# Performance work log

Hardware: AMD Instinct MI355X
Metric: run time of the kernel (lower is better)

The kernel has to match this reference:

```python
import jax, jax.numpy as jnp
import numpy as np

D_MODEL = 2048
N_HEAD = 16
SEM_DIM = 1024
GEO_DIM = 1024
ATTN_DIM = 2048
ROPE_BASE = 10000.0


def _rope(x, base=ROPE_BASE):
    # x: [B, H, S, d] with even d; GPT-NeoX rotate-half convention
    S, d = x.shape[-2], x.shape[-1]
    inv_freq = 1.0 / (base ** (jnp.arange(0, d, 2, dtype=jnp.float32) / d))
    t = jnp.arange(S, dtype=jnp.float32)
    freqs = jnp.einsum('s,f->sf', t, inv_freq)  # [S, d/2]
    cos, sin = jnp.cos(freqs), jnp.sin(freqs)
    x1, x2 = x[..., : d // 2], x[..., d // 2 :]
    return jnp.concatenate([x1 * cos - x2 * sin, x1 * sin + x2 * cos], axis=-1).astype(x.dtype)


def _split_heads(y, H):
    B, S, dim = y.shape
    return y.reshape(B, S, H, dim // H).transpose(0, 2, 1, 3)  # [B,H,S,hd]


def setup_inputs() -> dict:
    key = jax.random.key(0)
    ks = jax.random.split(key, 7)
    B, S = 2, 2048
    sd = 0.02
    return {
        'x': jax.random.normal(ks[0], (B, S, D_MODEL), dtype=jnp.float32),
        'Wq_sem': jax.random.normal(ks[1], (SEM_DIM, D_MODEL), dtype=jnp.float32) * sd,
        'Wk_sem': jax.random.normal(ks[2], (SEM_DIM, D_MODEL), dtype=jnp.float32) * sd,
        'Wq_geo': jax.random.normal(ks[3], (GEO_DIM, D_MODEL), dtype=jnp.float32) * sd,
        'Wk_geo': jax.random.normal(ks[4], (GEO_DIM, D_MODEL), dtype=jnp.float32) * sd,
        'Wv': jax.random.normal(ks[5], (ATTN_DIM, D_MODEL), dtype=jnp.float32) * sd,
        'Wo': jax.random.normal(ks[6], (D_MODEL, ATTN_DIM), dtype=jnp.float32) * sd,
    }


def reference(x, Wq_sem, Wk_sem, Wq_geo, Wk_geo, Wv, Wo):
    B, S, _ = x.shape
    H = N_HEAD
    # decoupled projections (nn.Linear: y = x @ W.T)
    q_sem = _split_heads(x @ Wq_sem.T, H)  # [B,H,S,64]
    k_sem = _split_heads(x @ Wk_sem.T, H)
    q_geo = _rope(_split_heads(x @ Wq_geo.T, H))  # RoPE only on geo part
    k_geo = _rope(_split_heads(x @ Wk_geo.T, H))
    v = _split_heads(x @ Wv.T, H)  # [B,H,S,128]
    # concatenated decoupled q/k -> single fused score (fp32), SDPA default scale
    q = jnp.concatenate([q_sem, q_geo], axis=-1)
    k = jnp.concatenate([k_sem, k_geo], axis=-1)
    scale = 1.0 / jnp.sqrt(jnp.asarray(q.shape[-1], dtype=jnp.float32))
    scores = jnp.einsum('bhqd,bhkd->bhqk', q, k).astype(jnp.float32) * scale
    causal = jnp.tril(jnp.ones((S, S), dtype=bool))
    scores = jnp.where(causal, scores, jnp.finfo(jnp.float32).min)
    attn = jax.nn.softmax(scores, axis=-1).astype(v.dtype)
    out = jnp.einsum('bhqk,bhkd->bhqd', attn, v)  # [B,H,S,128]
    out = out.transpose(0, 2, 1, 3).reshape(B, S, ATTN_DIM)
    return out @ Wo.T  # [B,S,d_model]
```

## Files before the change

kernel.cpp:

```cpp
#include <hip/hip_runtime.h>
#include <cstdint>
#include <cstddef>

typedef unsigned short u16;
typedef __attribute__((ext_vector_type(8))) short bf16x8;
typedef __attribute__((ext_vector_type(4))) float f32x4;

#define MFMA32(a, b, c) __builtin_amdgcn_mfma_f32_16x16x32_bf16(a, b, c, 0, 0, 0)

__device__ __forceinline__ u16 f2b(float f) {
  union { float f; unsigned u; } v; v.f = f;
  unsigned u = v.u;
  return (u16)((u + 0x7fffu + ((u >> 16) & 1u)) >> 16);
}
__device__ __forceinline__ float b2f(u16 h) {
  union { unsigned u; float f; } v; v.u = ((unsigned)h) << 16;
  return v.f;
}

__device__ __forceinline__ void g2l16(const void* g, void* l) {
  __builtin_amdgcn_global_load_lds((__attribute__((address_space(1))) void*)(g),
                                   (__attribute__((address_space(3))) void*)(l), 16, 0, 0);
}

__global__ __launch_bounds__(256) void cast_all(const float* __restrict__ x,
                                                const float* __restrict__ W0,
                                                const float* __restrict__ W1,
                                                const float* __restrict__ W2,
                                                const float* __restrict__ W3,
                                                const float* __restrict__ Wv,
                                                const float* __restrict__ Wo,
                                                u16* __restrict__ xb,
                                                u16* __restrict__ Wall,
                                                u16* __restrict__ Wob) {
  const int blk = blockIdx.x;
  const float* src;
  u16* dst;
  int li;
  if (blk < 8192) {
    src = x; dst = xb; li = blk * 256 + threadIdx.x;
  } else if (blk < 16384) {
    const int s = (blk - 8192) >> 11;
    src = s == 0 ? W0 : s == 1 ? W1 : s == 2 ? W2 : W3;
    dst = Wall + (size_t)s * 2097152;
    li = ((blk - 8192) & 2047) * 256 + threadIdx.x;
  } else if (blk < 20480) {
    src = Wv; dst = Wall + (size_t)4 * 2097152;
    li = (blk - 16384) * 256 + threadIdx.x;
  } else {
    src = Wo; dst = Wob;
    li = (blk - 20480) * 256 + threadIdx.x;
  }
  float4 v = ((const float4*)src)[li];
  ushort4 r;
  r.x = f2b(v.x); r.y = f2b(v.y); r.z = f2b(v.z); r.w = f2b(v.w);
  ((ushort4*)dst)[li] = r;
}

template <bool BF16_OUT>
__global__ __launch_bounds__(256) void gemm_bt(const u16* __restrict__ A,
                                               const u16* __restrict__ B,
                                               void* __restrict__ C, int N, int K) {
  __shared__ u16 As[128 * 64];
  __shared__ u16 Bs[128 * 64];
  const int tid = threadIdx.x;
  const int wid = tid >> 6;
  const int lane = tid & 63;
  const int lm = lane & 15;
  const int quad = lane >> 4;
  const int r3 = lm & 7;
  const int wm = (wid & 1) * 64;
  const int wn = (wid >> 1) * 64;
  const int bm = blockIdx.y * 128;
  const int bn = blockIdx.x * 128;

  const u16* Ab = A + (size_t)bm * K;
  const u16* Bb = B + (size_t)bn * K;

  f32x4 zero = {0.f, 0.f, 0.f, 0.f};
  f32x4 acc[4][4];
#pragma unroll
  for (int i = 0; i < 4; ++i)
#pragma unroll
    for (int j = 0; j < 4; ++j) acc[i][j] = zero;

  for (int k0 = 0; k0 < K; k0 += 64) {
#pragma unroll
    for (int it = 0; it < 4; ++it) {
      int c = it * 256 + tid;
      int rg = c >> 6, rw = (c >> 3) & 7, u = c & 7;
      int row = rg * 8 + rw;
      int chd = u ^ rw;
      g2l16(Ab + (size_t)row * K + k0 + chd * 8, As + c * 8);
      g2l16(Bb + (size_t)row * K + k0 + chd * 8, Bs + c * 8);
    }
    __syncthreads();
#pragma unroll
    for (int ks = 0; ks < 2; ++ks) {
      bf16x8 a[4], b[4];
      int chd = ks * 4 + quad;
#pragma unroll
      for (int i = 0; i < 4; ++i) {
        int row = wm + i * 16 + lm;
        a[i] = *(const bf16x8*)(As + (((row >> 3) * 64 + r3 * 8 + (chd ^ r3)) * 8));
      }
#pragma unroll
      for (int j = 0; j < 4; ++j) {
        int row = wn + j * 16 + lm;
        b[j] = *(const bf16x8*)(Bs + (((row >> 3) * 64 + r3 * 8 + (chd ^ r3)) * 8));
      }
#pragma unroll
      for (int i = 0; i < 4; ++i)
#pragma unroll
        for (int j = 0; j < 4; ++j)
          acc[i][j] = MFMA32(a[i], b[j], acc[i][j]);
    }
    __syncthreads();
  }

#pragma unroll
  for (int i = 0; i < 4; ++i)
#pragma unroll
    for (int j = 0; j < 4; ++j)
#pragma unroll
      for (int r = 0; r < 4; ++r) {
        int row = bm + wm + i * 16 + quad * 4 + r;
        int col = bn + wn + j * 16 + lm;
        float v = acc[i][j][r];
        if (BF16_OUT)
          ((u16*)C)[(size_t)row * N + col] = f2b(v);
        else
          ((float*)C)[(size_t)row * N + col] = v;
      }
}

__global__ __launch_bounds__(256) void gemm_qkv(const u16* __restrict__ A,
                                                const u16* __restrict__ B,
                                                u16* __restrict__ Qb,
                                                u16* __restrict__ Kb,
                                                u16* __restrict__ VT) {
  constexpr int K = 2048;
  const float SC = 0.12751744f;
  __shared__ u16 sh[16384];
  u16* As = sh;
  u16* Bs = sh + 8192;
  const int tid = threadIdx.x;
  const int wid = tid >> 6;
  const int lane = tid & 63;
  const int lm = lane & 15;
  const int quad = lane >> 4;
  const int r3 = lm & 7;
  const int wm = (wid & 1) * 64;
  const int wn = (wid >> 1) * 64;
  const int bm = blockIdx.y * 128;
  const int bn = blockIdx.x * 128;

  const u16* Ab = A + (size_t)bm * K;
  const u16* Bb = B + (size_t)bn * K;

  f32x4 zero = {0.f, 0.f, 0.f, 0.f};
  f32x4 acc[4][4];
#pragma unroll
  for (int i = 0; i < 4; ++i)
#pragma unroll
    for (int j = 0; j < 4; ++j) acc[i][j] = zero;

  for (int k0 = 0; k0 < K; k0 += 64) {
#pragma unroll
    for (int it = 0; it < 4; ++it) {
      int c = it * 256 + tid;
      int rg = c >> 6, rw = (c >> 3) & 7, u = c & 7;
      int row = rg * 8 + rw;
      int chd = u ^ rw;
      g2l16(Ab + (size_t)row * K + k0 + chd * 8, As + c * 8);
      g2l16(Bb + (size_t)row * K + k0 + chd * 8, Bs + c * 8);
    }
    __syncthreads();
#pragma unroll
    for (int ks = 0; ks < 2; ++ks) {
      bf16x8 a[4], b[4];
      int chd = ks * 4 + quad;
#pragma unroll
      for (int i = 0; i < 4; ++i) {
        int row = wm + i * 16 + lm;
        a[i] = *(const bf16x8*)(As + (((row >> 3) * 64 + r3 * 8 + (chd ^ r3)) * 8));
      }
#pragma unroll
      for (int j = 0; j < 4; ++j) {
        int row = wn + j * 16 + lm;
        b[j] = *(const bf16x8*)(Bs + (((row >> 3) * 64 + r3 * 8 + (chd ^ r3)) * 8));
      }
#pragma unroll
      for (int i = 0; i < 4; ++i)
#pragma unroll
        for (int j = 0; j < 4; ++j)
          acc[i][j] = MFMA32(a[i], b[j], acc[i][j]);
    }
    __syncthreads();
  }

  const int seg = bn >> 10;
  const int b = bm >> 11;
  const int sbase = bm & 2047;
  const int h = ((bn + wn) >> 6) & 15;
  const size_t bhQ = (size_t)b * 16 + h;

  if (seg < 2) {
    u16* dst = (seg == 0) ? Qb : Kb;
    const float sc = (seg == 0) ? SC : 1.0f;
#pragma unroll
    for (int i = 0; i < 4; ++i)
#pragma unroll
      for (int r = 0; r < 4; ++r) {
        const int s = sbase + wm + i * 16 + quad * 4 + r;
        u16* base = dst + (bhQ * 2048 + s) * 128;
#pragma unroll
        for (int j = 0; j < 4; ++j) {
          const int d = (wn + j * 16 + lm) & 63;
          base[d] = f2b(acc[i][j][r] * sc);
        }
      }
  } else if (seg < 4) {
    u16* dst = (seg == 2) ? Qb : Kb;
    const float sc = (seg == 2) ? SC : 1.0f;
    const float inv0 = __powf(10000.0f, -(float)(2 * lm) * (1.0f / 64.0f));
    const float inv1 = __powf(10000.0f, -(float)(2 * (16 + lm)) * (1.0f / 64.0f));
#pragma unroll
    for (int i = 0; i < 4; ++i)
#pragma unroll
      for (int r = 0; r < 4; ++r) {
        const int s = sbase + wm + i * 16 + quad * 4 + r;
        float sn0, cs0, sn1, cs1;
        __sincosf((float)s * inv0, &sn0, &cs0);
        __sincosf((float)s * inv1, &sn1, &cs1);
        const float x1a = acc[i][0][r], x2a = acc[i][2][r];
        const float x1b = acc[i][1][r], x2b = acc[i][3][r];
        u16* base = dst + (bhQ * 2048 + s) * 128 + 64;
        base[lm]      = f2b((x1a * cs0 - x2a * sn0) * sc);
        base[16 + lm] = f2b((x1b * cs1 - x2b * sn1) * sc);
        base[32 + lm] = f2b((x1a * sn0 + x2a * cs0) * sc);
        base[48 + lm] = f2b((x1b * sn1 + x2b * cs1) * sc);
      }
  } else {
    const int hv = (bn - 4096) >> 7;
    const size_t bh = (size_t)b * 16 + hv;
#pragma unroll
    for (int i = 0; i < 4; ++i)
#pragma unroll
      for (int r = 0; r < 4; ++r) {
        const int sr = wm + i * 16 + quad * 4 + r;
#pragma unroll
        for (int j = 0; j < 4; ++j) {
          const int d = wn + j * 16 + lm;
          sh[d * 128 + (((sr >> 3) ^ (d & 7)) << 3) + (sr & 7)] = f2b(acc[i][j][r]);
        }
      }
    __syncthreads();
#pragma unroll
    for (int it = 0; it < 8; ++it) {
      const int idx = it * 256 + tid;
      const int d = idx >> 4;
      const int ch = idx & 15;
      bf16x8 v = *(const bf16x8*)(sh + d * 128 + ((ch ^ (d & 7)) << 3));
      *(bf16x8*)(VT + (bh * 128 + d) * 2048 + sbase + ch * 8) = v;
    }
  }
}

__global__ __launch_bounds__(256, 3) void attn_v9(const u16* __restrict__ Q,
                                                  const u16* __restrict__ K,
                                                  const u16* __restrict__ VT,
                                                  u16* __restrict__ O) {
  constexpr int S = 2048;
  constexpr int D = 128;
  __shared__ u16 Ks[64 * 128];
  __shared__ u16 Vs[128 * 64];
  __shared__ u16 Ps[64 * 72];
  const int linear = blockIdx.x + (blockIdx.y << 4);
  const int xcd = linear & 7;
  const int slot = linear >> 3;
  const int bh = (xcd << 2) + (slot >> 4);
  const int bx = slot & 15;
  const int b = bh >> 4, h = bh & 15;
  const int tid = threadIdx.x, wid = tid >> 6, lane = tid & 63;
  const int lm = lane & 15, quad = lane >> 4;
  const int rx = lm & 7;
  const int wrow = wid * 16;

  const u16* Kbh = K + (size_t)bh * S * D;
  const u16* Vbh = VT + (size_t)bh * D * S;

  const bf16x8 vones = {16256, 16256, 16256, 16256, 16256, 16256, 16256, 16256};

#pragma unroll 1
  for (int pass = 0; pass < 2; ++pass) {
    const int qt = pass == 0 ? bx : 31 - bx;

    bf16x8 aq[4];
#pragma unroll
    for (int ks = 0; ks < 4; ++ks)
      aq[ks] = *(const bf16x8*)(Q + ((size_t)bh * S + (size_t)qt * 64 + wrow + lm) * D +
                                ks * 32 + quad * 8);

    f32x4 zero = {0.f, 0.f, 0.f, 0.f};
    f32x4 lsum = zero;
    f32x4 oacc[8];
#pragma unroll
    for (int t = 0; t < 8; ++t) oacc[t] = zero;

#pragma unroll 1
    for (int kt = 0; kt <= qt; ++kt) {
      __syncthreads();
      const u16* Kt = Kbh + (size_t)kt * 64 * D;
      const u16* Vt = Vbh + (size_t)kt * 64;
#pragma unroll
      for (int it = 0; it < 4; ++it) {
        int c = it * 256 + tid;
        int row = c >> 4, u = c & 15;
        g2l16(Kt + (size_t)row * 128 + (size_t)(u ^ (row & 7)) * 8, Ks + c * 8);
      }
#pragma unroll
      for (int it = 0; it < 4; ++it) {
        int c = it * 256 + tid;
        int row = c >> 3, u = c & 7;
        g2l16(Vt + (size_t)row * S + (size_t)(u ^ (row & 7)) * 8, Vs + c * 8);
      }
      __syncthreads();

      f32x4 sc[4];
#pragma unroll
      for (int j = 0; j < 4; ++j) sc[j] = zero;
      __builtin_amdgcn_s_setprio(1);
#pragma unroll
      for (int ks = 0; ks < 4; ++ks) {
        const int kc = ks * 4 + quad;
#pragma unroll
        for (int j = 0; j < 4; ++j) {
          bf16x8 bk = *(const bf16x8*)(Ks + (((j * 16 + lm) * 16 + (kc ^ rx)) * 8));
          sc[j] = MFMA32(aq[ks], bk, sc[j]);
        }
      }
      __builtin_amdgcn_s_setprio(0);

      const bool diag = (kt == qt);
#pragma unroll
      for (int r = 0; r < 4; ++r) {
        const int qcol = wrow + quad * 4 + r;
        const int prow = (wrow + quad * 4 + r) * 72;
#pragma unroll
        for (int j = 0; j < 4; ++j) {
          float p = __builtin_amdgcn_exp2f(fminf(sc[j][r], 30.0f));
          if (diag && (j * 16 + lm > qcol)) p = 0.f;
          Ps[prow + j * 16 + lm] = f2b(p);
        }
      }

      __builtin_amdgcn_s_setprio(1);
#pragma unroll
      for (int ks = 0; ks < 2; ++ks) {
        bf16x8 ap = *(const bf16x8*)(Ps + (wrow + lm) * 72 + ks * 32 + quad * 8);
        const int kc = ks * 4 + quad;
        lsum = MFMA32(ap, vones, lsum);
#pragma unroll
        for (int t = 0; t < 8; ++t) {
          bf16x8 bv = *(const bf16x8*)(Vs + (((t * 16 + lm) * 8 + (kc ^ rx)) * 8));
          oacc[t] = MFMA32(ap, bv, oacc[t]);
        }
      }
      __builtin_amdgcn_s_setprio(0);
    }

#pragma unroll
    for (int r = 0; r < 4; ++r) {
      float inv = 1.0f / lsum[r];
      const int srow = qt * 64 + wrow + quad * 4 + r;
      u16* Orow = O + ((size_t)b * S + srow) * 2048 + h * 128;
#pragma unroll
      for (int t = 0; t < 8; ++t) Orow[t * 16 + lm] = f2b(oacc[t][r] * inv);
    }
  }
}

extern "C" void kernel_launch(void* const* d_in, const int* in_sizes, int n_in,
                              void* d_out, int out_size, void* d_ws, size_t ws_size,
                              hipStream_t stream) {
  const float* x      = (const float*)d_in[0];
  const float* Wq_sem = (const float*)d_in[1];
  const float* Wk_sem = (const float*)d_in[2];
  const float* Wq_geo = (const float*)d_in[3];
  const float* Wk_geo = (const float*)d_in[4];
  const float* Wv     = (const float*)d_in[5];
  const float* Wo     = (const float*)d_in[6];

  char* ws = (char*)d_ws;
  u16* xb   = (u16*)(ws);
  u16* Wall = (u16*)(ws + 16777216);
  u16* Wob  = (u16*)(ws + 16777216 + 25165824);
  u16* Qb   = (u16*)(ws + 16777216 + 25165824 + 8388608);
  u16* Ob   = Wall;
  u16* Kb   = (u16*)d_out;
  u16* VT   = (u16*)((char*)d_out + 16777216);

  cast_all<<<24576, 256, 0, stream>>>(x, Wq_sem, Wk_sem, Wq_geo, Wk_geo, Wv, Wo,
                                      xb, Wall, Wob);

  gemm_qkv<<<dim3(48, 32), 256, 0, stream>>>(xb, Wall, Qb, Kb, VT);

  attn_v9<<<dim3(16, 32), 256, 0, stream>>>(Qb, Kb, VT, Ob);

  gemm_bt<false><<<dim3(16, 32), 256, 0, stream>>>(Ob, Wob, d_out, 2048, 2048);
}
```

Before: 359.4 us.

## Process both paired query tiles in one KV sweep to share K/V loads

The attention kernel used to make two sequential passes, one per query tile (bx and 31-bx), and reloaded the K/V tiles from global memory in each pass. Now a single loop over KV tiles serves both query tiles: the later tile B uses every KV tile and the earlier tile A only the tiles up to its causal limit, so each K/V tile is staged into LDS once. The cost is twice the accumulator registers (two sets of 8 f32x4 output accumulators plus two Q fragments) and a second P buffer in LDS, which under launch_bounds(256,3) may cause spills or lower occupancy.

```diff
diff --git a/kernel.cpp b/kernel.cpp
--- a/kernel.cpp
+++ b/kernel.cpp
@@ -267,15 +267,16 @@
   }
 }
 
-__global__ __launch_bounds__(256, 3) void attn_v9(const u16* __restrict__ Q,
-                                                  const u16* __restrict__ K,
-                                                  const u16* __restrict__ VT,
-                                                  u16* __restrict__ O) {
+__global__ __launch_bounds__(256, 3) void attn_v10(const u16* __restrict__ Q,
+                                                   const u16* __restrict__ K,
+                                                   const u16* __restrict__ VT,
+                                                   u16* __restrict__ O) {
   constexpr int S = 2048;
   constexpr int D = 128;
   __shared__ u16 Ks[64 * 128];
   __shared__ u16 Vs[128 * 64];
-  __shared__ u16 Ps[64 * 72];
+  __shared__ u16 PsA[64 * 72];
+  __shared__ u16 PsB[64 * 72];
   const int linear = blockIdx.x + (blockIdx.y << 4);
   const int xcd = linear & 7;
   const int slot = linear >> 3;
@@ -287,46 +288,51 @@
   const int rx = lm & 7;
   const int wrow = wid * 16;
 
+  const int qtA = bx;
+  const int qtB = 31 - bx;
+
   const u16* Kbh = K + (size_t)bh * S * D;
   const u16* Vbh = VT + (size_t)bh * D * S;
 
   const bf16x8 vones = {16256, 16256, 16256, 16256, 16256, 16256, 16256, 16256};
 
+  bf16x8 aqA[4], aqB[4];
+#pragma unroll
+  for (int ks = 0; ks < 4; ++ks) {
+    aqA[ks] = *(const bf16x8*)(Q + ((size_t)bh * S + (size_t)qtA * 64 + wrow + lm) * D +
+                               ks * 32 + quad * 8);
+    aqB[ks] = *(const bf16x8*)(Q + ((size_t)bh * S + (size_t)qtB * 64 + wrow + lm) * D +
+                               ks * 32 + quad * 8);
+  }
+
+  f32x4 zero = {0.f, 0.f, 0.f, 0.f};
+  f32x4 lsumA = zero, lsumB = zero;
+  f32x4 oaccA[8], oaccB[8];
+#pragma unroll
+  for (int t = 0; t < 8; ++t) { oaccA[t] = zero; oaccB[t] = zero; }
+
 #pragma unroll 1
-  for (int pass = 0; pass < 2; ++pass) {
-    const int qt = pass == 0 ? bx : 31 - bx;
-
-    bf16x8 aq[4];
-#pragma unroll
-    for (int ks = 0; ks < 4; ++ks)
-      aq[ks] = *(const bf16x8*)(Q + ((size_t)bh * S + (size_t)qt * 64 + wrow + lm) * D +
-                                ks * 32 + quad * 8);
-
-    f32x4 zero = {0.f, 0.f, 0.f, 0.f};
-    f32x4 lsum = zero;
-    f32x4 oacc[8];
-#pragma unroll
-    for (int t = 0; t < 8; ++t) oacc[t] = zero;
-
-#pragma unroll 1
-    for (int kt = 0; kt <= qt; ++kt) {
-      __syncthreads();
-      const u16* Kt = Kbh + (size_t)kt * 64 * D;
-      const u16* Vt = Vbh + (size_t)kt * 64;
-#pragma unroll
-      for (int it = 0; it < 4; ++it) {
-        int c = it * 256 + tid;
-        int row = c >> 4, u = c & 15;
-        g2l16(Kt + (size_t)row * 128 + (size_t)(u ^ (row & 7)) * 8, Ks + c * 8);
-      }
-#pragma unroll
-      for (int it = 0; it < 4; ++it) {
-        int c = it * 256 + tid;
-        int row = c >> 3, u = c & 7;
-        g2l16(Vt + (size_t)row * S + (size_t)(u ^ (row & 7)) * 8, Vs + c * 8);
-      }
-      __syncthreads();
-
+  for (int kt = 0; kt <= qtB; ++kt) {
+    __syncthreads();
+    const u16* Kt = Kbh + (size_t)kt * 64 * D;
+    const u16* Vt = Vbh + (size_t)kt * 64;
+#pragma unroll
+    for (int it = 0; it < 4; ++it) {
+      int c = it * 256 + tid;
+      int row = c >> 4, u = c & 15;
+      g2l16(Kt + (size_t)row * 128 + (size_t)(u ^ (row & 7)) * 8, Ks + c * 8);
+    }
+#pragma unroll
+    for (int it = 0; it < 4; ++it) {
+      int c = it * 256 + tid;
+      int row = c >> 3, u = c & 7;
+      g2l16(Vt + (size_t)row * S + (size_t)(u ^ (row & 7)) * 8, Vs + c * 8);
+    }
+    __syncthreads();
+
+    const bool doA = (kt <= qtA);
+
+    {
       f32x4 sc[4];
 #pragma unroll
       for (int j = 0; j < 4; ++j) sc[j] = zero;
@@ -337,12 +343,11 @@
 #pragma unroll
         for (int j = 0; j < 4; ++j) {
           bf16x8 bk = *(const bf16x8*)(Ks + (((j * 16 + lm) * 16 + (kc ^ rx)) * 8));
-          sc[j] = MFMA32(aq[ks], bk, sc[j]);
+          sc[j] = MFMA32(aqB[ks], bk, sc[j]);
         }
       }
       __builtin_amdgcn_s_setprio(0);
-
-      const bool diag = (kt == qt);
+      const bool diag = (kt == qtB);
 #pragma unroll
       for (int r = 0; r < 4; ++r) {
         const int qcol = wrow + quad * 4 + r;
@@ -351,32 +356,87 @@
         for (int j = 0; j < 4; ++j) {
           float p = __builtin_amdgcn_exp2f(fminf(sc[j][r], 30.0f));
           if (diag && (j * 16 + lm > qcol)) p = 0.f;
-          Ps[prow + j * 16 + lm] = f2b(p);
-        }
-      }
-
+          PsB[prow + j * 16 + lm] = f2b(p);
+        }
+      }
+    }
+
+    if (doA) {
+      f32x4 sc[4];
+#pragma unroll
+      for (int j = 0; j < 4; ++j) sc[j] = zero;
       __builtin_amdgcn_s_setprio(1);
 #pragma unroll
+      for (int ks = 0; ks < 4; ++ks) {
+        const int kc = ks * 4 + quad;
+#pragma unroll
+        for (int j = 0; j < 4; ++j) {
+          bf16x8 bk = *(const bf16x8*)(Ks + (((j * 16 + lm) * 16 + (kc ^ rx)) * 8));
+          sc[j] = MFMA32(aqA[ks], bk, sc[j]);
+        }
+      }
+      __builtin_amdgcn_s_setprio(0);
+      const bool diag = (kt == qtA);
+#pragma unroll
+      for (int r = 0; r < 4; ++r) {
+        const int qcol = wrow + quad * 4 + r;
+        const int prow = (wrow + quad * 4 + r) * 72;
+#pragma unroll
+        for (int j = 0; j < 4; ++j) {
+          float p = __builtin_amdgcn_exp2f(fminf(sc[j][r], 30.0f));
+          if (diag && (j * 16 + lm > qcol)) p = 0.f;
+          PsA[prow + j * 16 + lm] = f2b(p);
+        }
+      }
+    }
+
+    __builtin_amdgcn_s_setprio(1);
+#pragma unroll
+    for (int ks = 0; ks < 2; ++ks) {
+      bf16x8 ap = *(const bf16x8*)(PsB + (wrow + lm) * 72 + ks * 32 + quad * 8);
+      const int kc = ks * 4 + quad;
+      lsumB = MFMA32(ap, vones, lsumB);
+#pragma unroll
+      for (int t = 0; t < 8; ++t) {
+        bf16x8 bv = *(const bf16x8*)(Vs + (((t * 16 + lm) * 8 + (kc ^ rx)) * 8));
+        oaccB[t] = MFMA32(ap, bv, oaccB[t]);
+      }
+    }
+    __builtin_amdgcn_s_setprio(0);
+
+    if (doA) {
+      __builtin_amdgcn_s_setprio(1);
+#pragma unroll
       for (int ks = 0; ks < 2; ++ks) {
-        bf16x8 ap = *(const bf16x8*)(Ps + (wrow + lm) * 72 + ks * 32 + quad * 8);
+        bf16x8 ap = *(const bf16x8*)(PsA + (wrow + lm) * 72 + ks * 32 + quad * 8);
         const int kc = ks * 4 + quad;
-        lsum = MFMA32(ap, vones, lsum);
+        lsumA = MFMA32(ap, vones, lsumA);
 #pragma unroll
         for (int t = 0; t < 8; ++t) {
           bf16x8 bv = *(const bf16x8*)(Vs + (((t * 16 + lm) * 8 + (kc ^ rx)) * 8));
-          oacc[t] = MFMA32(ap, bv, oacc[t]);
+          oaccA[t] = MFMA32(ap, bv, oaccA[t]);
         }
       }
       __builtin_amdgcn_s_setprio(0);
     }
-
-#pragma unroll
-    for (int r = 0; r < 4; ++r) {
-      float inv = 1.0f / lsum[r];
-      const int srow = qt * 64 + wrow + quad * 4 + r;
+  }
+
+#pragma unroll
+  for (int r = 0; r < 4; ++r) {
+    const int rr = quad * 4 + r;
+    {
+      float inv = 1.0f / lsumA[r];
+      const int srow = qtA * 64 + wrow + rr;
       u16* Orow = O + ((size_t)b * S + srow) * 2048 + h * 128;
 #pragma unroll
-      for (int t = 0; t < 8; ++t) Orow[t * 16 + lm] = f2b(oacc[t][r] * inv);
+      for (int t = 0; t < 8; ++t) Orow[t * 16 + lm] = f2b(oaccA[t][r] * inv);
+    }
+    {
+      float inv = 1.0f / lsumB[r];
+      const int srow = qtB * 64 + wrow + rr;
+      u16* Orow = O + ((size_t)b * S + srow) * 2048 + h * 128;
+#pragma unroll
+      for (int t = 0; t < 8; ++t) Orow[t * 16 + lm] = f2b(oaccB[t][r] * inv);
     }
   }
 }
@@ -406,7 +466,7 @@
 
   gemm_qkv<<<dim3(48, 32), 256, 0, stream>>>(xb, Wall, Qb, Kb, VT);
 
-  attn_v9<<<dim3(16, 32), 256, 0, stream>>>(Qb, Kb, VT, Ob);
+  attn_v10<<<dim3(16, 32), 256, 0, stream>>>(Qb, Kb, VT, Ob);
 
   gemm_bt<false><<<dim3(16, 32), 256, 0, stream>>>(Ob, Wob, d_out, 2048, 2048);
 }
```

Result: no change. 359.3 us (-0.0%).

## Rewrite QKV GEMM as 8-wave 128x256 tile with double-buffered ping-pong pipeline

Applied to the files above, without the earlier changes.

The fused QKV projection GEMM moves from 4 waves on a 128x128 tile with a single-buffered LDS loop to 8 waves on a 128x256 tile. A/B tiles are double-buffered in 96KB of dynamic LDS. Global-to-LDS staging is interleaved with MFMA sub-blocks using fine-grained barriers, explicit vmcnt waits and s_setprio, so loads overlap compute. The V-transpose epilogue is adapted to cover two heads per block. This adds more LDS and barriers per block, which lowers occupancy and brings some synchronization risk.

```diff
diff --git a/kernel.cpp b/kernel.cpp
--- a/kernel.cpp
+++ b/kernel.cpp
@@ -134,29 +134,25 @@
       }
 }
 
-__global__ __launch_bounds__(256) void gemm_qkv(const u16* __restrict__ A,
-                                                const u16* __restrict__ B,
-                                                u16* __restrict__ Qb,
-                                                u16* __restrict__ Kb,
-                                                u16* __restrict__ VT) {
+__global__ __launch_bounds__(512, 2) void gemm_qkv8(const u16* __restrict__ A,
+                                                    const u16* __restrict__ B,
+                                                    u16* __restrict__ Qb,
+                                                    u16* __restrict__ Kb,
+                                                    u16* __restrict__ VT) {
   constexpr int K = 2048;
   const float SC = 0.12751744f;
-  __shared__ u16 sh[16384];
-  u16* As = sh;
-  u16* Bs = sh + 8192;
+  extern __shared__ u16 sh[];
+  u16* sA = sh;
+  u16* sB = sh + 16384;
   const int tid = threadIdx.x;
-  const int wid = tid >> 6;
-  const int lane = tid & 63;
-  const int lm = lane & 15;
-  const int quad = lane >> 4;
-  const int r3 = lm & 7;
-  const int wm = (wid & 1) * 64;
-  const int wn = (wid >> 1) * 64;
+  const int wid = tid >> 6, lane = tid & 63;
+  const int lm = lane & 15, quad = lane >> 4, rx = lm & 7;
+  const int wm = (wid >> 2) * 64;
+  const int wn = (wid & 3) * 64;
   const int bm = blockIdx.y * 128;
-  const int bn = blockIdx.x * 128;
-
-  const u16* Ab = A + (size_t)bm * K;
-  const u16* Bb = B + (size_t)bn * K;
+  const int bn = blockIdx.x * 256;
+  const u16* Ablk = A + (size_t)bm * K;
+  const u16* Bblk = B + (size_t)bn * K;
 
   f32x4 zero = {0.f, 0.f, 0.f, 0.f};
   f32x4 acc[4][4];
@@ -165,38 +161,113 @@
 #pragma unroll
     for (int j = 0; j < 4; ++j) acc[i][j] = zero;
 
-  for (int k0 = 0; k0 < K; k0 += 64) {
-#pragma unroll
-    for (int it = 0; it < 4; ++it) {
-      int c = it * 256 + tid;
-      int rg = c >> 6, rw = (c >> 3) & 7, u = c & 7;
-      int row = rg * 8 + rw;
-      int chd = u ^ rw;
-      g2l16(Ab + (size_t)row * K + k0 + chd * 8, As + c * 8);
-      g2l16(Bb + (size_t)row * K + k0 + chd * 8, Bs + c * 8);
-    }
-    __syncthreads();
-#pragma unroll
-    for (int ks = 0; ks < 2; ++ks) {
-      bf16x8 a[4], b[4];
-      int chd = ks * 4 + quad;
-#pragma unroll
-      for (int i = 0; i < 4; ++i) {
-        int row = wm + i * 16 + lm;
-        a[i] = *(const bf16x8*)(As + (((row >> 3) * 64 + r3 * 8 + (chd ^ r3)) * 8));
-      }
-#pragma unroll
-      for (int j = 0; j < 4; ++j) {
-        int row = wn + j * 16 + lm;
-        b[j] = *(const bf16x8*)(Bs + (((row >> 3) * 64 + r3 * 8 + (chd ^ r3)) * 8));
-      }
-#pragma unroll
-      for (int i = 0; i < 4; ++i)
-#pragma unroll
-        for (int j = 0; j < 4; ++j)
-          acc[i][j] = MFMA32(a[i], b[j], acc[i][j]);
-    }
-    __syncthreads();
+  bf16x8 aA[2][2];
+  bf16x8 bB[2][2][2];
+
+  auto stageu = [&](int st, int ut) {
+    const int k0 = st << 6;
+    const int bf = st & 1;
+    const u16* src;
+    u16* dst;
+    int rowbase;
+    if (ut == 0) { src = Ablk; rowbase = 0; dst = sA + bf * 8192; }
+    else { src = Bblk; rowbase = (ut - 1) << 7; dst = sB + bf * 16384 + ((ut - 1) << 13); }
+#pragma unroll
+    for (int it = 0; it < 2; ++it) {
+      const int c = it * 512 + tid;
+      const int r = c >> 3, u = c & 7;
+      g2l16(src + (size_t)(rowbase + r) * K + k0 + ((u ^ (r & 7)) << 3), dst + (size_t)c * 8);
+    }
+  };
+  auto ldA = [&](int bf, int mh) {
+    const u16* base = sA + bf * 8192;
+#pragma unroll
+    for (int ii = 0; ii < 2; ++ii)
+#pragma unroll
+      for (int ks = 0; ks < 2; ++ks) {
+        const int row = wm + mh * 32 + ii * 16 + lm;
+        aA[ii][ks] = *(const bf16x8*)(base + ((row * 8 + ((ks * 4 + quad) ^ rx)) << 3));
+      }
+  };
+  auto ldB = [&](int bf, int nh) {
+    const u16* base = sB + bf * 16384;
+#pragma unroll
+    for (int jj = 0; jj < 2; ++jj)
+#pragma unroll
+      for (int ks = 0; ks < 2; ++ks) {
+        const int row = wn + nh * 32 + jj * 16 + lm;
+        bB[nh][jj][ks] = *(const bf16x8*)(base + ((row * 8 + ((ks * 4 + quad) ^ rx)) << 3));
+      }
+  };
+  auto mm = [&](int mh, int nh) {
+    __builtin_amdgcn_s_setprio(1);
+#pragma unroll
+    for (int ii = 0; ii < 2; ++ii)
+#pragma unroll
+      for (int jj = 0; jj < 2; ++jj)
+#pragma unroll
+        for (int ks = 0; ks < 2; ++ks)
+          acc[mh * 2 + ii][nh * 2 + jj] =
+              MFMA32(aA[ii][ks], bB[nh][jj][ks], acc[mh * 2 + ii][nh * 2 + jj]);
+    __builtin_amdgcn_s_setprio(0);
+  };
+
+  const int NT = K >> 6;
+  const int NIT = NT >> 1;
+
+  stageu(0, 0); stageu(0, 1); stageu(0, 2); stageu(1, 0);
+  asm volatile("s_waitcnt vmcnt(2)" ::: "memory");
+  __builtin_amdgcn_s_barrier();
+
+#pragma unroll 1
+  for (int i = 0; i < NIT; ++i) {
+    const int t1 = 2 * i + 1, t2 = 2 * i + 2, t3 = 2 * i + 3;
+    ldA(0, 0); ldB(0, 0);
+    stageu(t1, 1);
+    __builtin_amdgcn_s_barrier();
+    mm(0, 0);
+    __builtin_amdgcn_s_barrier();
+    ldB(0, 1);
+    stageu(t1, 2);
+    __builtin_amdgcn_s_barrier();
+    mm(0, 1);
+    __builtin_amdgcn_s_barrier();
+    ldA(0, 1);
+    __builtin_amdgcn_s_barrier();
+    mm(1, 1);
+    __builtin_amdgcn_s_barrier();
+    {
+      const bool st = (t2 < NT);
+      if (st) stageu(t2, 0);
+      __builtin_amdgcn_s_barrier();
+      mm(1, 0);
+      if (st) asm volatile("s_waitcnt vmcnt(2)" ::: "memory");
+      else    asm volatile("s_waitcnt vmcnt(0)" ::: "memory");
+      __builtin_amdgcn_s_barrier();
+    }
+    ldA(1, 0); ldB(1, 0);
+    if (t2 < NT) stageu(t2, 1);
+    __builtin_amdgcn_s_barrier();
+    mm(0, 0);
+    __builtin_amdgcn_s_barrier();
+    ldB(1, 1);
+    if (t2 < NT) stageu(t2, 2);
+    __builtin_amdgcn_s_barrier();
+    mm(0, 1);
+    __builtin_amdgcn_s_barrier();
+    ldA(1, 1);
+    __builtin_amdgcn_s_barrier();
+    mm(1, 1);
+    __builtin_amdgcn_s_barrier();
+    {
+      const bool st = (t3 < NT);
+      if (st) stageu(t3, 0);
+      __builtin_amdgcn_s_barrier();
+      mm(1, 0);
+      if (st) asm volatile("s_waitcnt vmcnt(2)" ::: "memory");
+      else    asm volatile("s_waitcnt vmcnt(0)" ::: "memory");
+      __builtin_amdgcn_s_barrier();
+    }
   }
 
   const int seg = bn >> 10;
@@ -242,8 +313,7 @@
         base[48 + lm] = f2b((x1b * sn1 + x2b * cs1) * sc);
       }
   } else {
-    const int hv = (bn - 4096) >> 7;
-    const size_t bh = (size_t)b * 16 + hv;
+    const int hv0 = (bn - 4096) >> 7;
 #pragma unroll
     for (int i = 0; i < 4; ++i)
 #pragma unroll
@@ -258,11 +328,12 @@
     __syncthreads();
 #pragma unroll
     for (int it = 0; it < 8; ++it) {
-      const int idx = it * 256 + tid;
+      const int idx = it * 512 + tid;
       const int d = idx >> 4;
       const int ch = idx & 15;
       bf16x8 v = *(const bf16x8*)(sh + d * 128 + ((ch ^ (d & 7)) << 3));
-      *(bf16x8*)(VT + (bh * 128 + d) * 2048 + sbase + ch * 8) = v;
+      const size_t bh = (size_t)b * 16 + hv0 + (d >> 7);
+      *(bf16x8*)(VT + (bh * 128 + (d & 127)) * 2048 + sbase + ch * 8) = v;
     }
   }
 }
@@ -401,10 +472,13 @@
   u16* Kb   = (u16*)d_out;
   u16* VT   = (u16*)((char*)d_out + 16777216);
 
+  hipFuncSetAttribute((const void*)gemm_qkv8,
+                      hipFuncAttributeMaxDynamicSharedMemorySize, 98304);
+
   cast_all<<<24576, 256, 0, stream>>>(x, Wq_sem, Wk_sem, Wq_geo, Wk_geo, Wv, Wo,
                                       xb, Wall, Wob);
 
-  gemm_qkv<<<dim3(48, 32), 256, 0, stream>>>(xb, Wall, Qb, Kb, VT);
+  gemm_qkv8<<<dim3(24, 32), 512, 98304, stream>>>(xb, Wall, Qb, Kb, VT);
 
   attn_v9<<<dim3(16, 32), 256, 0, stream>>>(Qb, Kb, VT, Ob);
 
```

Result: faster. 338.4 us (-5.8%).
